# Kernel tuning notes

Measured on AMD Instinct MI355X. Metric: run time of the kernel, lower is better.

Reference implementation:

```python
import jax, jax.numpy as jnp
import numpy as np

EMBD = 512
HEADS = 8
HEAD = EMBD // HEADS


def setup_inputs() -> dict:
    key = jax.random.key(0)
    ks = jax.random.split(key, 9)
    B, M = 4, 2048
    s = 1.0 / np.sqrt(EMBD)
    inp = {
        "x": jax.random.normal(ks[0], (B, M, EMBD), dtype=jnp.float32),
        "wq": jax.random.uniform(ks[1], (EMBD, EMBD), jnp.float32, -s, s),
        "bq": jnp.zeros((EMBD,), jnp.float32),
        "wk": jax.random.uniform(ks[2], (EMBD, EMBD), jnp.float32, -s, s),
        "bk": jnp.zeros((EMBD,), jnp.float32),
        "wv": jax.random.uniform(ks[3], (EMBD, EMBD), jnp.float32, -s, s),
        "bv": jnp.zeros((EMBD,), jnp.float32),
        "wo": jax.random.uniform(ks[4], (EMBD, EMBD), jnp.float32, -s, s),
        "bo": jnp.zeros((EMBD,), jnp.float32),
        "gamma": jnp.ones((EMBD,), jnp.float32),
        "beta": jnp.zeros((EMBD,), jnp.float32),
    }
    return inp


def layer_norm(x, gamma, beta, eps=1e-5):
    mu = jnp.mean(x, axis=-1, keepdims=True)
    var = jnp.mean(jnp.square(x - mu), axis=-1, keepdims=True)
    return (x - mu) * jax.lax.rsqrt(var + eps) * gamma + beta


def reference(x, wq, bq, wk, bk, wv, bv, wo, bo, gamma, beta):
    B, M, _ = x.shape
    norm = layer_norm(x, gamma, beta)
    # projections; reshape to [B, H, M, Dh]
    def proj(w, b):
        return (norm @ w.T + b).reshape(B, M, HEADS, HEAD).transpose(0, 2, 1, 3)
    q = proj(wq, bq)
    k = proj(wk, bk)
    v = proj(wv, bv)
    scores = jnp.einsum("bhmd,bhnd->bhmn", q, k) / np.sqrt(HEAD)
    # exclude self-attention on the diagonal
    diag = jnp.eye(M, dtype=bool)
    scores = jnp.where(diag, -jnp.inf, scores)
    attn = jax.nn.softmax(scores, axis=-1)
    ctx = jnp.einsum("bhmn,bhnd->bhmd", attn, v)
    ctx = ctx.transpose(0, 2, 1, 3).reshape(B, M, EMBD)
    out = ctx @ wo.T + bo
    return (out + x, attn)
```

## Files before the change

kernel.cpp:

```cpp
#include <hip/hip_runtime.h>

#define B_   4
#define H_   8
#define M_   2048
#define D_   512
#define DH_  64

typedef short  bf16x8 __attribute__((ext_vector_type(8)));
typedef short  bf16x4 __attribute__((ext_vector_type(4)));
typedef float  f32x4  __attribute__((ext_vector_type(4)));
typedef unsigned short u16x4 __attribute__((ext_vector_type(4)));
typedef unsigned int   u32x2 __attribute__((ext_vector_type(2)));

#define EXPC 0.18033688011112042f

static __device__ __forceinline__ unsigned short f2bf(float f) {
  unsigned u = __float_as_uint(f);
  u += 0x7fffu + ((u >> 16) & 1u);
  return (unsigned short)(u >> 16);
}

static __device__ __forceinline__ unsigned cvtpk(float lo, float hi) {
  unsigned r;
  asm("v_cvt_pk_bf16_f32 %0, %1, %2" : "=v"(r) : "v"(lo), "v"(hi));
  return r;
}

static __device__ __forceinline__ f32x4 mfma16(bf16x4 a, bf16x4 b, f32x4 c) {
  asm("v_mfma_f32_16x16x16_bf16 %0, %1, %2, %0" : "+v"(c) : "v"(a), "v"(b));
  return c;
}

static __device__ __forceinline__ int swz128(int row, int byteoff) {
  return row * 128 + (byteoff ^ ((row & 7) << 4));
}

static __device__ __forceinline__ void glds16(const void* g, void* l) {
  __builtin_amdgcn_global_load_lds(
      (const __attribute__((address_space(1))) unsigned*)g,
      (__attribute__((address_space(3))) unsigned*)l, 16, 0, 0);
}

static __device__ __forceinline__ void stage_tile(
    const char* g0, size_t rstride, char* lds, int t) {
  const int r0 = t >> 3, c0 = t & 7;
  const char* src = g0 + (size_t)r0 * rstride + ((c0 ^ (r0 & 7)) << 4);
  char* dst = lds + ((t & 192) << 4);
  #pragma unroll
  for (int c = 0; c < 4; ++c)
    glds16(src + (size_t)c * 32 * rstride, dst + c * 4096);
}

__global__ __launch_bounds__(256) void ln_kernel(
    const float* __restrict__ x, const float* __restrict__ gamma,
    const float* __restrict__ beta, unsigned short* __restrict__ xn)
{
  int row = blockIdx.x;
  int t = threadIdx.x;
  const float* xr = x + (size_t)row * D_;
  float v0 = xr[t], v1 = xr[t + 256];
  float s = v0 + v1, ss = v0 * v0 + v1 * v1;
  #pragma unroll
  for (int m = 1; m < 64; m <<= 1) {
    s  += __shfl_xor(s, m);
    ss += __shfl_xor(ss, m);
  }
  __shared__ float red[8];
  int wid = t >> 6;
  if ((t & 63) == 0) { red[wid] = s; red[wid + 4] = ss; }
  __syncthreads();
  s  = red[0] + red[1] + red[2] + red[3];
  ss = red[4] + red[5] + red[6] + red[7];
  float mu  = s * (1.0f / D_);
  float var = ss * (1.0f / D_) - mu * mu;
  float rstd = rsqrtf(var + 1e-5f);
  unsigned short* o = xn + (size_t)row * D_;
  o[t]       = f2bf((v0 - mu) * rstd * gamma[t]       + beta[t]);
  o[t + 256] = f2bf((v1 - mu) * rstd * gamma[t + 256] + beta[t + 256]);
}

__global__ __launch_bounds__(256) void cast_w_kernel(
    const float* __restrict__ wq, const float* __restrict__ wk,
    const float* __restrict__ wv, const float* __restrict__ wo,
    unsigned short* __restrict__ wqkv, unsigned short* __restrict__ wob)
{
  int i = blockIdx.x * 256 + threadIdx.x;
  wqkv[i]          = f2bf(wq[i]);
  wqkv[i + 262144] = f2bf(wk[i]);
  wqkv[i + 524288] = f2bf(wv[i]);
  wob[i]           = f2bf(wo[i]);
}

__global__ __launch_bounds__(256) void qkv_gemm(
    const unsigned short* __restrict__ xn,
    const unsigned short* __restrict__ wqkv,
    const float* __restrict__ bq, const float* __restrict__ bk,
    const float* __restrict__ bv,
    unsigned short* __restrict__ q, unsigned short* __restrict__ Kp,
    unsigned short* __restrict__ Vp)
{
  __shared__ __align__(16) char As[128 * 128];
  __shared__ __align__(16) char Bs[128 * 128];
  const int m0 = blockIdx.x * 128;
  const int n0 = blockIdx.y * 128;
  const int t = threadIdx.x, wid = t >> 6, lane = t & 63;
  const int wr = (wid >> 1) * 64, wc = (wid & 1) * 64;
  const int cl = lane & 15, rg = lane >> 4;
  const f32x4 z4 = {0.f, 0.f, 0.f, 0.f};
  const bool isv = (n0 >= 1024);

  const char* agb = (const char*)xn   + (size_t)m0 * 1024;
  const char* bgb = (const char*)wqkv + (size_t)n0 * 1024;

  f32x4 acc[4][4];
  #pragma unroll
  for (int i = 0; i < 4; ++i)
    #pragma unroll
    for (int j = 0; j < 4; ++j) acc[i][j] = z4;

  for (int k0 = 0; k0 < 512; k0 += 64) {
    __syncthreads();
    stage_tile(agb + k0 * 2, 1024, As, t);
    stage_tile(bgb + k0 * 2, 1024, Bs, t);
    __syncthreads();
    #pragma unroll
    for (int ks = 0; ks < 2; ++ks) {
      int koff = ks * 64 + rg * 16;
      bf16x8 af[4], bfr[4];
      #pragma unroll
      for (int i = 0; i < 4; ++i)
        af[i] = *(const bf16x8*)(As + swz128(wr + i * 16 + cl, koff));
      #pragma unroll
      for (int j = 0; j < 4; ++j)
        bfr[j] = *(const bf16x8*)(Bs + swz128(wc + j * 16 + cl, koff));
      if (isv) {
        #pragma unroll
        for (int i = 0; i < 4; ++i)
          #pragma unroll
          for (int j = 0; j < 4; ++j)
            acc[i][j] = __builtin_amdgcn_mfma_f32_16x16x32_bf16(af[i], bfr[j], acc[i][j], 0, 0, 0);
      } else {
        #pragma unroll
        for (int j = 0; j < 4; ++j)
          #pragma unroll
          for (int i = 0; i < 4; ++i)
            acc[j][i] = __builtin_amdgcn_mfma_f32_16x16x32_bf16(bfr[j], af[i], acc[j][i], 0, 0, 0);
      }
    }
  }

  if (isv) {
    #pragma unroll
    for (int j = 0; j < 4; ++j) {
      int n = n0 + wc + j * 16 + cl;
      int nn = n & 511;
      int h = nn >> 6, dh = nn & 63;
      int jd = dh >> 4, cld = dh & 15;
      float bias = bv[nn];
      #pragma unroll
      for (int i = 0; i < 4; ++i) {
        int mrow = m0 + wr + i * 16 + rg * 4;
        int b = mrow >> 11, mm = mrow & 2047;
        int nt = mm >> 6, nl = mm & 63;
        int jp = nl >> 5, half = (nl >> 4) & 1, rgv = (nl >> 2) & 3;
        u32x2 u;
        u[0] = cvtpk(acc[i][j][0] + bias, acc[i][j][1] + bias);
        u[1] = cvtpk(acc[i][j][2] + bias, acc[i][j][3] + bias);
        size_t off = ((((size_t)(b * H_ + h) * 32 + nt) * 4 + jd) * 2 + jp) * 512
                   + (rgv * 16 + cld) * 8 + half * 4;
        *(u16x4*)(Vp + off) = __builtin_bit_cast(u16x4, u);
      }
    }
  } else {
    const int mat = n0 >> 9;
    #pragma unroll
    for (int j = 0; j < 4; ++j) {
      int nn0 = ((n0 + wc) & 511) + j * 16 + rg * 4;
      int h = nn0 >> 6, dh = nn0 & 63;
      f32x4 b4 = *(const f32x4*)((mat ? bk : bq) + nn0);
      #pragma unroll
      for (int i = 0; i < 4; ++i) {
        int mrow = m0 + wr + i * 16 + cl;
        int b = mrow >> 11, mm = mrow & 2047;
        u32x2 u;
        u[0] = cvtpk(acc[j][i][0] + b4[0], acc[j][i][1] + b4[1]);
        u[1] = cvtpk(acc[j][i][2] + b4[2], acc[j][i][3] + b4[3]);
        if (mat == 0) {
          *(u16x4*)(q + ((size_t)(b * H_ + h) * M_ + mm) * DH_ + dh) =
              __builtin_bit_cast(u16x4, u);
        } else {
          int ks = dh >> 5, rgk = (dh >> 3) & 3, e0 = dh & 7;
          size_t off = ((((size_t)(b * H_ + h) * 32 + (mm >> 6)) * 4 + ((mm >> 4) & 3)) * 2 + ks) * 512
                     + (rgk * 16 + (mm & 15)) * 8 + e0;
          *(u16x4*)(Kp + off) = __builtin_bit_cast(u16x4, u);
        }
      }
    }
  }
}

__global__ __launch_bounds__(256, 4) void attn_kernel(
    const unsigned short* __restrict__ q,
    const unsigned short* __restrict__ Kp,
    const unsigned short* __restrict__ Vp,
    float* __restrict__ attn,
    unsigned short* __restrict__ ctx)
{
  __shared__ __align__(16) char Ps[4][2048];

  const int flat = blockIdx.x;
  const int bh = (flat & 7) * 4 + ((flat >> 3) >> 5);
  const int mb = (flat >> 3) & 31;
  const int m0 = mb * 64;
  const int t = threadIdx.x, wid = t >> 6, lane = t & 63;
  const int wr = wid * 16, cl = lane & 15, rg = lane >> 4;
  const int m_g = m0 + wr + cl;
  const f32x4 z4 = {0.f, 0.f, 0.f, 0.f};

  const char* qb = (const char*)(q + (size_t)bh * M_ * DH_);
  const unsigned short* kpb = Kp + (size_t)bh * 131072;
  const unsigned short* vpb = Vp + (size_t)bh * 131072;
  float* ab = attn + (size_t)bh * M_ * M_;

  bf16x8 qf[2];
  #pragma unroll
  for (int ks = 0; ks < 2; ++ks)
    qf[ks] = *(const bf16x8*)(qb + (size_t)m_g * 128 + ks * 64 + rg * 16);

  float psum = 0.f;
  for (int nt = 0; nt < 32; ++nt) {
    const unsigned short* kch = kpb + (size_t)nt * 4096;
    f32x4 s[4];
    #pragma unroll
    for (int j = 0; j < 4; ++j) s[j] = z4;
    #pragma unroll
    for (int ks = 0; ks < 2; ++ks)
      #pragma unroll
      for (int j = 0; j < 4; ++j) {
        bf16x8 kf = *(const bf16x8*)(kch + (j * 2 + ks) * 512 + lane * 8);
        s[j] = __builtin_amdgcn_mfma_f32_16x16x32_bf16(kf, qf[ks], s[j], 0, 0, 0);
      }
    if (nt == mb) {
      #pragma unroll
      for (int j = 0; j < 4; ++j)
        #pragma unroll
        for (int r = 0; r < 4; ++r) {
          int n_g = nt * 64 + j * 16 + rg * 4 + r;
          float p = __builtin_amdgcn_exp2f(s[j][r] * EXPC);
          psum += (n_g == m_g) ? 0.f : p;
        }
    } else {
      #pragma unroll
      for (int j = 0; j < 4; ++j)
        #pragma unroll
        for (int r = 0; r < 4; ++r)
          psum += __builtin_amdgcn_exp2f(s[j][r] * EXPC);
    }
  }
  psum += __shfl_xor(psum, 16);
  psum += __shfl_xor(psum, 32);
  const float rv = 1.0f / psum;

  f32x4 oc[4];
  #pragma unroll
  for (int j = 0; j < 4; ++j) oc[j] = z4;

  const int srow = lane >> 4;
  const int sch  = lane & 15;

  asm volatile("s_nop 7" :::);

  for (int nt = 0; nt < 32; ++nt) {
    const unsigned short* kch = kpb + (size_t)nt * 4096;
    const unsigned short* vch = vpb + (size_t)nt * 4096;
    f32x4 s[4];
    #pragma unroll
    for (int j = 0; j < 4; ++j) s[j] = z4;
    #pragma unroll
    for (int ks = 0; ks < 2; ++ks)
      #pragma unroll
      for (int j = 0; j < 4; ++j) {
        bf16x8 kf = *(const bf16x8*)(kch + (j * 2 + ks) * 512 + lane * 8);
        s[j] = __builtin_amdgcn_mfma_f32_16x16x32_bf16(kf, qf[ks], s[j], 0, 0, 0);
      }
    const bool dtile = (nt == mb);
    bf16x4 pb[4];
    #pragma unroll
    for (int j = 0; j < 4; ++j) {
      f32x4 pv;
      #pragma unroll
      for (int r = 0; r < 4; ++r) {
        int n_g = nt * 64 + j * 16 + rg * 4 + r;
        float p = __builtin_amdgcn_exp2f(s[j][r] * EXPC) * rv;
        pv[r] = (dtile && n_g == m_g) ? 0.f : p;
      }
      u32x2 u;
      u[0] = cvtpk(pv[0], pv[1]);
      u[1] = cvtpk(pv[2], pv[3]);
      pb[j] = __builtin_bit_cast(bf16x4, u);
      *(u32x2*)(Ps[wid] + swz128(cl, j * 32 + rg * 8)) = u;
    }
    {
      float* abase = ab + ((size_t)(m0 + wr + srow)) * M_ + nt * 64 + sch * 4;
      #pragma unroll
      for (int it = 0; it < 4; ++it) {
        u16x4 pu = *(const u16x4*)(Ps[wid] + swz128(it * 4 + srow, sch * 8));
        f32x4 pv;
        #pragma unroll
        for (int r = 0; r < 4; ++r) pv[r] = __uint_as_float((unsigned)pu[r] << 16);
        __builtin_nontemporal_store(pv, (f32x4*)(abase + (size_t)it * 4 * M_));
      }
    }
    #pragma unroll
    for (int jp = 0; jp < 2; ++jp)
      #pragma unroll
      for (int jd = 0; jd < 4; ++jd) {
        bf16x8 w = *(const bf16x8*)(vch + (jd * 2 + jp) * 512 + lane * 8);
        bf16x4 vlo = __builtin_shufflevector(w, w, 0, 1, 2, 3);
        bf16x4 vhi = __builtin_shufflevector(w, w, 4, 5, 6, 7);
        oc[jd] = mfma16(vlo, pb[jp * 2],     oc[jd]);
        oc[jd] = mfma16(vhi, pb[jp * 2 + 1], oc[jd]);
      }
  }

  asm volatile("s_nop 7\n\ts_nop 7" :::);

  int b = bh >> 3, h = bh & 7;
  unsigned short* crow = ctx + ((size_t)b * M_ + m_g) * D_ + h * DH_ + rg * 4;
  #pragma unroll
  for (int jd = 0; jd < 4; ++jd) {
    u32x2 u;
    u[0] = cvtpk(oc[jd][0], oc[jd][1]);
    u[1] = cvtpk(oc[jd][2], oc[jd][3]);
    *(u32x2*)(crow + jd * 16) = u;
  }
}

__global__ __launch_bounds__(256) void out_gemm(
    const unsigned short* __restrict__ ctxb,
    const unsigned short* __restrict__ wob,
    const float* __restrict__ bo,
    const float* __restrict__ x,
    float* __restrict__ out)
{
  __shared__ __align__(16) char As[128 * 128];
  __shared__ __align__(16) char Bs[128 * 128];
  const int m0 = blockIdx.x * 128;
  const int n0 = blockIdx.y * 128;
  const int t = threadIdx.x, wid = t >> 6, lane = t & 63;
  const int wr = (wid >> 1) * 64, wc = (wid & 1) * 64;
  const int cl = lane & 15, rg = lane >> 4;
  const f32x4 z4 = {0.f, 0.f, 0.f, 0.f};

  const char* agb = (const char*)ctxb + (size_t)m0 * 1024;
  const char* bgb = (const char*)wob  + (size_t)n0 * 1024;

  f32x4 acc[4][4];
  #pragma unroll
  for (int j = 0; j < 4; ++j)
    #pragma unroll
    for (int i = 0; i < 4; ++i) acc[j][i] = z4;

  for (int k0 = 0; k0 < 512; k0 += 64) {
    __syncthreads();
    stage_tile(agb + k0 * 2, 1024, As, t);
    stage_tile(bgb + k0 * 2, 1024, Bs, t);
    __syncthreads();
    #pragma unroll
    for (int ks = 0; ks < 2; ++ks) {
      int koff = ks * 64 + rg * 16;
      bf16x8 af[4], bfr[4];
      #pragma unroll
      for (int i = 0; i < 4; ++i)
        af[i] = *(const bf16x8*)(As + swz128(wr + i * 16 + cl, koff));
      #pragma unroll
      for (int j = 0; j < 4; ++j)
        bfr[j] = *(const bf16x8*)(Bs + swz128(wc + j * 16 + cl, koff));
      #pragma unroll
      for (int j = 0; j < 4; ++j)
        #pragma unroll
        for (int i = 0; i < 4; ++i)
          acc[j][i] = __builtin_amdgcn_mfma_f32_16x16x32_bf16(bfr[j], af[i], acc[j][i], 0, 0, 0);
    }
  }

  #pragma unroll
  for (int j = 0; j < 4; ++j) {
    int nb = n0 + wc + j * 16 + rg * 4;
    f32x4 bo4 = *(const f32x4*)(bo + nb);
    #pragma unroll
    for (int i = 0; i < 4; ++i) {
      int m = m0 + wr + i * 16 + cl;
      f32x4 x4 = *(const f32x4*)(x + (size_t)m * 512 + nb);
      f32x4 o;
      #pragma unroll
      for (int r = 0; r < 4; ++r) o[r] = acc[j][i][r] + bo4[r] + x4[r];
      *(f32x4*)(out + (size_t)m * 512 + nb) = o;
    }
  }
}

extern "C" void kernel_launch(void* const* d_in, const int* in_sizes, int n_in,
                              void* d_out, int out_size, void* d_ws, size_t ws_size,
                              hipStream_t stream) {
  const float* x     = (const float*)d_in[0];
  const float* wq    = (const float*)d_in[1];
  const float* bq    = (const float*)d_in[2];
  const float* wk    = (const float*)d_in[3];
  const float* bk    = (const float*)d_in[4];
  const float* wv    = (const float*)d_in[5];
  const float* bv    = (const float*)d_in[6];
  const float* wo    = (const float*)d_in[7];
  const float* bo    = (const float*)d_in[8];
  const float* gamma = (const float*)d_in[9];
  const float* beta  = (const float*)d_in[10];

  char* ws = (char*)d_ws;
  unsigned short* xn   = (unsigned short*)(ws);
  unsigned short* wqkv = (unsigned short*)(ws + 8388608);
  unsigned short* wob  = (unsigned short*)(ws + 9961472);
  unsigned short* qb   = (unsigned short*)(ws + 10485760);
  unsigned short* Kp   = (unsigned short*)(ws + 18874368);
  unsigned short* Vp   = (unsigned short*)(ws + 27262976);
  unsigned short* ctx  = (unsigned short*)(ws + 35651584);

  float* out  = (float*)d_out;
  float* attn = (float*)d_out + 4194304;

  ln_kernel<<<8192, 256, 0, stream>>>(x, gamma, beta, xn);
  cast_w_kernel<<<1024, 256, 0, stream>>>(wq, wk, wv, wo, wqkv, wob);
  qkv_gemm<<<dim3(64, 12), 256, 0, stream>>>(xn, wqkv, bq, bk, bv, qb, Kp, Vp);
  attn_kernel<<<1024, 256, 0, stream>>>(qb, Kp, Vp, attn, ctx);
  out_gemm<<<dim3(64, 4), 256, 0, stream>>>(ctx, wob, bo, x, out);
}
```

Baseline: 201.6 us.

## Vectorize layernorm, store attn directly from registers, shrink out_gemm N tile

The layernorm kernel now processes two rows per block with float4 loads and packed bf16 stores. The attention kernel drops the LDS round-trip used to transpose the bf16 probabilities. It instead writes fp32 probabilities straight from the MFMA output layout and folds the 1/sum normalisation into the exponent. Each thread now writes four 16-byte chunks scattered across rows, which may coalesce worse. The stored attn values are no longer rounded through bf16. The output GEMM uses 64-wide N tiles, doubling the grid for better CU occupancy.

```diff
diff --git a/kernel.cpp b/kernel.cpp
--- a/kernel.cpp
+++ b/kernel.cpp
@@ -51,32 +51,52 @@
     glds16(src + (size_t)c * 32 * rstride, dst + c * 4096);
 }
 
+static __device__ __forceinline__ void stage64(
+    const char* g0, size_t rstride, char* lds, int t) {
+  #pragma unroll
+  for (int c = 0; c < 2; ++c) {
+    int s = c * 256 + t;
+    int row = s >> 3, ch = s & 7;
+    const char* src = g0 + (size_t)row * rstride + ((ch ^ (row & 7)) << 4);
+    glds16(src, lds + c * 4096 + ((t & 192) << 4));
+  }
+}
+
 __global__ __launch_bounds__(256) void ln_kernel(
     const float* __restrict__ x, const float* __restrict__ gamma,
     const float* __restrict__ beta, unsigned short* __restrict__ xn)
 {
-  int row = blockIdx.x;
-  int t = threadIdx.x;
-  const float* xr = x + (size_t)row * D_;
-  float v0 = xr[t], v1 = xr[t + 256];
-  float s = v0 + v1, ss = v0 * v0 + v1 * v1;
+  const int t = threadIdx.x;
+  const int half = t >> 7;
+  const int i = t & 127;
+  const int row = blockIdx.x * 2 + half;
+
+  f32x4 v = *(const f32x4*)(x + (size_t)row * D_ + i * 4);
+  float s  = v[0] + v[1] + v[2] + v[3];
+  float ss = v[0]*v[0] + v[1]*v[1] + v[2]*v[2] + v[3]*v[3];
   #pragma unroll
   for (int m = 1; m < 64; m <<= 1) {
     s  += __shfl_xor(s, m);
     ss += __shfl_xor(ss, m);
   }
-  __shared__ float red[8];
-  int wid = t >> 6;
-  if ((t & 63) == 0) { red[wid] = s; red[wid + 4] = ss; }
+  __shared__ float red[2][2][2];
+  const int w = (i >> 6) & 1;
+  if ((i & 63) == 0) { red[half][w][0] = s; red[half][w][1] = ss; }
   __syncthreads();
-  s  = red[0] + red[1] + red[2] + red[3];
-  ss = red[4] + red[5] + red[6] + red[7];
+  s  = red[half][0][0] + red[half][1][0];
+  ss = red[half][0][1] + red[half][1][1];
   float mu  = s * (1.0f / D_);
   float var = ss * (1.0f / D_) - mu * mu;
   float rstd = rsqrtf(var + 1e-5f);
-  unsigned short* o = xn + (size_t)row * D_;
-  o[t]       = f2bf((v0 - mu) * rstd * gamma[t]       + beta[t]);
-  o[t + 256] = f2bf((v1 - mu) * rstd * gamma[t + 256] + beta[t + 256]);
+
+  f32x4 g4 = *(const f32x4*)(gamma + i * 4);
+  f32x4 b4 = *(const f32x4*)(beta  + i * 4);
+  u32x2 u;
+  u[0] = cvtpk((v[0] - mu) * rstd * g4[0] + b4[0],
+               (v[1] - mu) * rstd * g4[1] + b4[1]);
+  u[1] = cvtpk((v[2] - mu) * rstd * g4[2] + b4[2],
+               (v[3] - mu) * rstd * g4[3] + b4[3]);
+  *(u32x2*)(xn + (size_t)row * D_ + i * 4) = u;
 }
 
 __global__ __launch_bounds__(256) void cast_w_kernel(
@@ -206,8 +226,6 @@
     float* __restrict__ attn,
     unsigned short* __restrict__ ctx)
 {
-  __shared__ __align__(16) char Ps[4][2048];
-
   const int flat = blockIdx.x;
   const int bh = (flat & 7) * 4 + ((flat >> 3) >> 5);
   const int mb = (flat >> 3) & 31;
@@ -259,14 +277,11 @@
   }
   psum += __shfl_xor(psum, 16);
   psum += __shfl_xor(psum, 32);
-  const float rv = 1.0f / psum;
+  const float lrv = -__log2f(psum);
 
   f32x4 oc[4];
   #pragma unroll
   for (int j = 0; j < 4; ++j) oc[j] = z4;
-
-  const int srow = lane >> 4;
-  const int sch  = lane & 15;
 
   asm volatile("s_nop 7" :::);
 
@@ -285,31 +300,21 @@
       }
     const bool dtile = (nt == mb);
     bf16x4 pb[4];
+    float* arow = ab + (size_t)m_g * M_ + nt * 64 + rg * 4;
     #pragma unroll
     for (int j = 0; j < 4; ++j) {
       f32x4 pv;
       #pragma unroll
       for (int r = 0; r < 4; ++r) {
         int n_g = nt * 64 + j * 16 + rg * 4 + r;
-        float p = __builtin_amdgcn_exp2f(s[j][r] * EXPC) * rv;
+        float p = __builtin_amdgcn_exp2f(__builtin_fmaf(s[j][r], EXPC, lrv));
         pv[r] = (dtile && n_g == m_g) ? 0.f : p;
       }
-      u32x2 u;
-      u[0] = cvtpk(pv[0], pv[1]);
-      u[1] = cvtpk(pv[2], pv[3]);
-      pb[j] = __builtin_bit_cast(bf16x4, u);
-      *(u32x2*)(Ps[wid] + swz128(cl, j * 32 + rg * 8)) = u;
-    }
-    {
-      float* abase = ab + ((size_t)(m0 + wr + srow)) * M_ + nt * 64 + sch * 4;
-      #pragma unroll
-      for (int it = 0; it < 4; ++it) {
-        u16x4 pu = *(const u16x4*)(Ps[wid] + swz128(it * 4 + srow, sch * 8));
-        f32x4 pv;
-        #pragma unroll
-        for (int r = 0; r < 4; ++r) pv[r] = __uint_as_float((unsigned)pu[r] << 16);
-        __builtin_nontemporal_store(pv, (f32x4*)(abase + (size_t)it * 4 * M_));
-      }
+      __builtin_nontemporal_store(pv, (f32x4*)(arow + j * 16));
+      u32x2 uu;
+      uu[0] = cvtpk(pv[0], pv[1]);
+      uu[1] = cvtpk(pv[2], pv[3]);
+      pb[j] = __builtin_bit_cast(bf16x4, uu);
     }
     #pragma unroll
     for (int jp = 0; jp < 2; ++jp)
@@ -344,40 +349,40 @@
     float* __restrict__ out)
 {
   __shared__ __align__(16) char As[128 * 128];
-  __shared__ __align__(16) char Bs[128 * 128];
+  __shared__ __align__(16) char Bs[64 * 128];
   const int m0 = blockIdx.x * 128;
-  const int n0 = blockIdx.y * 128;
+  const int n0 = blockIdx.y * 64;
   const int t = threadIdx.x, wid = t >> 6, lane = t & 63;
-  const int wr = (wid >> 1) * 64, wc = (wid & 1) * 64;
+  const int wr = (wid >> 1) * 64, wc = (wid & 1) * 32;
   const int cl = lane & 15, rg = lane >> 4;
   const f32x4 z4 = {0.f, 0.f, 0.f, 0.f};
 
   const char* agb = (const char*)ctxb + (size_t)m0 * 1024;
   const char* bgb = (const char*)wob  + (size_t)n0 * 1024;
 
-  f32x4 acc[4][4];
-  #pragma unroll
-  for (int j = 0; j < 4; ++j)
+  f32x4 acc[2][4];
+  #pragma unroll
+  for (int j = 0; j < 2; ++j)
     #pragma unroll
     for (int i = 0; i < 4; ++i) acc[j][i] = z4;
 
   for (int k0 = 0; k0 < 512; k0 += 64) {
     __syncthreads();
     stage_tile(agb + k0 * 2, 1024, As, t);
-    stage_tile(bgb + k0 * 2, 1024, Bs, t);
+    stage64(bgb + k0 * 2, 1024, Bs, t);
     __syncthreads();
     #pragma unroll
     for (int ks = 0; ks < 2; ++ks) {
       int koff = ks * 64 + rg * 16;
-      bf16x8 af[4], bfr[4];
+      bf16x8 af[4], bfr[2];
       #pragma unroll
       for (int i = 0; i < 4; ++i)
         af[i] = *(const bf16x8*)(As + swz128(wr + i * 16 + cl, koff));
       #pragma unroll
-      for (int j = 0; j < 4; ++j)
+      for (int j = 0; j < 2; ++j)
         bfr[j] = *(const bf16x8*)(Bs + swz128(wc + j * 16 + cl, koff));
       #pragma unroll
-      for (int j = 0; j < 4; ++j)
+      for (int j = 0; j < 2; ++j)
         #pragma unroll
         for (int i = 0; i < 4; ++i)
           acc[j][i] = __builtin_amdgcn_mfma_f32_16x16x32_bf16(bfr[j], af[i], acc[j][i], 0, 0, 0);
@@ -385,7 +390,7 @@
   }
 
   #pragma unroll
-  for (int j = 0; j < 4; ++j) {
+  for (int j = 0; j < 2; ++j) {
     int nb = n0 + wc + j * 16 + rg * 4;
     f32x4 bo4 = *(const f32x4*)(bo + nb);
     #pragma unroll
@@ -427,9 +432,9 @@
   float* out  = (float*)d_out;
   float* attn = (float*)d_out + 4194304;
 
-  ln_kernel<<<8192, 256, 0, stream>>>(x, gamma, beta, xn);
+  ln_kernel<<<4096, 256, 0, stream>>>(x, gamma, beta, xn);
   cast_w_kernel<<<1024, 256, 0, stream>>>(wq, wk, wv, wo, wqkv, wob);
   qkv_gemm<<<dim3(64, 12), 256, 0, stream>>>(xn, wqkv, bq, bk, bv, qb, Kp, Vp);
   attn_kernel<<<1024, 256, 0, stream>>>(qb, Kp, Vp, attn, ctx);
-  out_gemm<<<dim3(64, 4), 256, 0, stream>>>(ctx, wob, bo, x, out);
-}
+  out_gemm<<<dim3(64, 8), 256, 0, stream>>>(ctx, wob, bo, x, out);
+}
```

Result: slower. 269.0 us (+33.4%).
